# Performance work log

Measured on AMD Instinct MI355X. Metric: run time of the kernel, lower is better.

The kernel has to match this reference:

```python
import jax, jax.numpy as jnp
import numpy as np

# Dimensions pinned by the module: RelPosEmb1DAISummer(tokens=50, dim_head=124)
H = 8          # num_heads
D = 31         # channels // num_heads
T = 4          # time axis of the (p, t) spatial grid; D*T == 124 == dim_head
P = 50         # tokens
C = H * D      # 248 channels
SCALE = D ** -0.5  # note: module scales by d**-0.5 (=31), not (d*t)**-0.5 -- faithful


def rel_to_abs(x):
    """AI-Summer 1D relative->absolute reindexing. x: [b, h, l, 2l-1] -> [b, h, l, l]."""
    b, h, l, _ = x.shape
    x = jnp.pad(x, ((0, 0), (0, 0), (0, 0), (0, 1)))          # [b,h,l,2l]
    x = x.reshape(b, h, l * 2 * l)
    x = jnp.pad(x, ((0, 0), (0, 0), (0, l - 1)))
    x = x.reshape(b, h, l + 1, 2 * l - 1)
    return x[:, :, :l, l - 1:]


def setup_inputs() -> dict:
    key = jax.random.key(0)
    k1, k2, k3, k4 = jax.random.split(key, 4)
    B = 512
    x = jax.random.normal(k1, (B, C, P, T), jnp.float32)
    # 1x1 conv == per-position linear over channels: weight [3C, C], bias [3C]
    w_qkv = jax.random.normal(k2, (3 * C, C), jnp.float32) * (C ** -0.5)
    b_qkv = jax.random.normal(k3, (3 * C,), jnp.float32) * 0.01
    # shared-heads relative position embedding: [2*tokens-1, dim_head]
    rel_emb = jax.random.normal(k4, (2 * P - 1, D * T), jnp.float32) * ((D * T) ** -0.5)
    return {"x": x, "w_qkv": w_qkv, "b_qkv": b_qkv, "rel_emb": rel_emb}


def reference(x, w_qkv, b_qkv, rel_emb):
    B = x.shape[0]
    # 1x1 Conv2d: [B, C, P, T] -> [B, 3C, P, T]
    qkv = jnp.einsum('bcpt,oc->bopt', x, w_qkv) + b_qkv[None, :, None, None]
    # 'b (qkv h d) p t -> qkv b h d p t'
    qkv = qkv.reshape(B, 3, H, D, P, T)
    q, k, v = qkv[:, 0], qkv[:, 1], qkv[:, 2]                 # each [B,H,D,P,T]
    q = q.transpose(0, 1, 3, 2, 4).reshape(B, H, P, D * T)    # 'b h d p t -> b h p (d t)'
    k = k.transpose(0, 1, 2, 4, 3).reshape(B, H, D * T, P)    # 'b h d p t -> b h (d t) p'
    v = v.transpose(0, 1, 3, 2, 4).reshape(B, H, P, D * T)
    dots = jnp.einsum('bhpi,bhiq->bhpq', q, k)                # [B,H,P,P]
    bias = rel_to_abs(jnp.einsum('bhpd,rd->bhpr', q, rel_emb))
    attn = jax.nn.softmax((dots + bias) * SCALE, axis=-1)     # dropout = identity (eval)
    out = jnp.einsum('bhpq,bhqi->bhpi', attn, v)              # [B,H,P,D*T]
    # 'b h p (d t) -> b (h d) p t'
    out = out.reshape(B, H, P, D, T).transpose(0, 1, 3, 2, 4).reshape(B, H * D, P, T)
    return out
```

## Files before the change

kernel.cpp:

```cpp
#include <hip/hip_runtime.h>
#include <hip/hip_bf16.h>
#include <stdint.h>

typedef __bf16 bf16_t;
typedef bf16_t bf16x8 __attribute__((ext_vector_type(8)));
typedef bf16_t bf16x4 __attribute__((ext_vector_type(4)));
typedef float f32x4 __attribute__((ext_vector_type(4)));

constexpr float SCALE = 0.17960530202677491f;

__device__ __forceinline__ f32x4 mfma16(bf16x8 a, bf16x8 b, f32x4 c) {
    return __builtin_amdgcn_mfma_f32_16x16x32_bf16(a, b, c, 0, 0, 0);
}
__device__ __forceinline__ void fence() {
    asm volatile("s_waitcnt lgkmcnt(0)" ::: "memory");
}
__device__ __forceinline__ void gload_lds16(const void* g, void* l) {
    __builtin_amdgcn_global_load_lds((const __attribute__((address_space(1))) void*)g,
                                     (__attribute__((address_space(3))) void*)l, 16, 0, 0);
}

__global__ void prep_kernel(const float* __restrict__ w, const float* __restrict__ rel,
                            bf16_t* __restrict__ WT, bf16_t* __restrict__ relf)
{
    int i = blockIdx.x * 256 + threadIdx.x;
    if (i < 196608) {
        int o = i >> 8, c = i & 255;
        WT[i] = (o < 744 && c < 248) ? (bf16_t)w[(long)o * 248 + c] : (bf16_t)0.f;
        return;
    }
    i -= 196608;
    if (i < 14336) {
        int e = i & 7, lane = (i >> 3) & 63;
        int f = i >> 9;
        int ks = f & 3, rt = f >> 2;
        int r = rt * 16 + (lane & 15);
        int dt = ks * 32 + (lane >> 4) * 8 + e;
        float v = 0.f;
        if (r < 99 && dt < 124) v = rel[r * 124 + dt];
        relf[i] = (bf16_t)v;
    }
}

__global__ void __launch_bounds__(512)
xb_kernel(const float* __restrict__ x, bf16_t* __restrict__ XT)
{
    __shared__ __align__(16) char XS[31744];
    const int tid = threadIdx.x;
    const int blk = blockIdx.x;
    const int cl = tid & 63;
    const int cg = tid >> 6;
    {
        int f = blk * 64 + cl;
        int b = f / 200;
        int nn = f - b * 200;
        const float* xp = x + (long)b * 49600 + nn;
#pragma unroll
        for (int ii = 0; ii < 4; ++ii) {
            int cb = cg + 8 * ii;
            if (cb < 31) {
                bf16x8 pk;
#pragma unroll
                for (int e = 0; e < 8; ++e)
                    pk[e] = (bf16_t)xp[(long)(cb * 8 + e) * 200];
                *(bf16x8*)(XS + cl * 496 + cb * 16) = pk;
            }
        }
    }
    __syncthreads();
    if (tid < 496) {
        char* dst = (char*)XT + (long)blk * 31744 + tid * 64;
#pragma unroll
        for (int j = 0; j < 4; ++j)
            *(f32x4*)(dst + j * 16) = *(const f32x4*)(XS + tid * 64 + j * 16);
    }
}

__global__ void __launch_bounds__(256)
qkv_kernel(const bf16_t* __restrict__ XT, const bf16_t* __restrict__ WT,
           const float* __restrict__ bqkv, bf16_t* __restrict__ qk,
           bf16_t* __restrict__ vbuf)
{
    __shared__ __align__(16) char SM[16384];
    const int raw = blockIdx.x;
    const int swz = (raw & 7) * 600 + (raw >> 3);
    const int mt = swz % 6, nt = swz / 6;
    const int n0 = nt * 128, o0 = mt * 128;
    const int tid  = threadIdx.x;
    const int lane = tid & 63;
    const int wv   = tid >> 6;
    const int r15  = lane & 15, g4 = lane >> 4;
    const int kc   = lane & 3, rsub = lane >> 2;
    const int wr = wv >> 1, wc = wv & 1;

    f32x4 acc[4][4];
#pragma unroll
    for (int a = 0; a < 4; ++a)
#pragma unroll
        for (int b = 0; b < 4; ++b) acc[a][b] = f32x4{0.f, 0.f, 0.f, 0.f};

    const char* XTb = (const char*)XT;
    const char* WTb = (const char*)WT;

#define STAGE(BUF, KS)                                                          \
    {                                                                           \
        _Pragma("unroll")                                                       \
        for (int i_ = 0; i_ < 2; ++i_) {                                        \
            int r0 = (wv * 2 + i_) * 16;                                        \
            int row = r0 + rsub;                                                \
            gload_lds16(XTb + (long)(n0 + row) * 496 + ((KS) * 4 + kc) * 16,    \
                        SM + (BUF) * 8192 + r0 * 64);                           \
        }                                                                       \
    }

    STAGE(0, 0);
    __syncthreads();

    int buf = 0;
    for (int ks = 0; ks < 8; ++ks) {
        if (ks < 7) STAGE(buf ^ 1, ks + 1);
        bf16x8 Af[4], Bf[4];
#pragma unroll
        for (int fo = 0; fo < 4; ++fo) {
            int row = wc * 64 + fo * 16 + r15;
            Bf[fo] = *(const bf16x8*)(WTb + (long)(o0 + row) * 512 + (ks * 4 + g4) * 16);
        }
#pragma unroll
        for (int fn = 0; fn < 4; ++fn) {
            int row = wr * 64 + fn * 16 + r15;
            Af[fn] = *(const bf16x8*)(SM + buf * 8192 + row * 64 + g4 * 16);
        }
#pragma unroll
        for (int fn = 0; fn < 4; ++fn)
#pragma unroll
            for (int fo = 0; fo < 4; ++fo)
                acc[fn][fo] = mfma16(Af[fn], Bf[fo], acc[fn][fo]);
        __syncthreads();
        buf ^= 1;
    }
#undef STAGE

#pragma unroll
    for (int fo = 0; fo < 4; ++fo) {
        int o = o0 + wc * 64 + fo * 16 + r15;
        bool vo = (o < 744);
        int s = (o >= 496) ? 2 : ((o >= 248) ? 1 : 0);
        int rem = o - s * 248;
        int h = rem / 31;
        int d = rem - h * 31;
        float bias = vo ? bqkv[o] : 0.f;
        float sc = (s == 0) ? SCALE : 1.f;
#pragma unroll
        for (int fn = 0; fn < 4; ++fn) {
            int n = n0 + wr * 64 + fn * 16 + g4 * 4;
            int b = n / 200;
            int p = (n - b * 200) >> 2;
            long bh = (long)(b * 8 + h);
            if (vo) {
                f32x4 a = acc[fn][fo];
                bf16x4 pk = {(bf16_t)((a[0] + bias) * sc), (bf16_t)((a[1] + bias) * sc),
                             (bf16_t)((a[2] + bias) * sc), (bf16_t)((a[3] + bias) * sc)};
                if (s < 2)
                    *(bf16x4*)(qk + (long)s * 26214400 + (bh * 50 + p) * 128 + d * 4) = pk;
                else
                    *(bf16x4*)(vbuf + bh * 8192 + p * 128 + d * 4) = pk;
            }
        }
    }
}

__global__ void __launch_bounds__(256)
attn_kernel(const bf16_t* __restrict__ qk, const bf16_t* __restrict__ vbuf,
            const bf16_t* __restrict__ relf, float* __restrict__ out)
{
    __shared__ float LS[50][52];
    __shared__ __align__(16) char AS[8192];
    __shared__ __align__(16) char VT[16384];
    __shared__ float RS[64];
    const int bid = blockIdx.x;
    const int bb = bid >> 3, hh = bid & 7;
    const int tid  = threadIdx.x;
    const int lane = tid & 63;
    const int w    = tid >> 6;
    const int r15  = lane & 15, g4 = lane >> 4;

    const bf16_t* qB = qk + (long)bid * 6400;
    const bf16_t* kB = qk + 26214400L + (long)bid * 6400;
    const bf16_t* vB = vbuf + (long)bid * 8192;

    {
        int p_ = tid >> 2, cc = tid & 3;
#pragma unroll
        for (int u = 0; u < 4; ++u) {
            int c = cc + u * 4;
            bf16x8 vv = *(const bf16x8*)(vB + p_ * 128 + c * 8);
#pragma unroll
            for (int e = 0; e < 8; ++e) {
                int i = c * 8 + e;
                *(bf16_t*)(VT + i * 128 + (((p_ >> 3) ^ (i & 7)) << 4) + (p_ & 7) * 2) = vv[e];
            }
        }
    }

    bf16x8 Afr[4];
#pragma unroll
    for (int ks = 0; ks < 4; ++ks)
        Afr[ks] = *(const bf16x8*)(qB + (w * 16 + r15) * 128 + ks * 32 + g4 * 8);

#pragma unroll
    for (int ct = 0; ct < 4; ++ct) {
        int c = ct * 16 + r15;
        f32x4 sA = f32x4{0.f, 0.f, 0.f, 0.f};
#pragma unroll
        for (int ks = 0; ks < 4; ++ks) {
            bf16x8 Bf = *(const bf16x8*)(kB + c * 128 + ks * 32 + g4 * 8);
            sA = mfma16(Afr[ks], Bf, sA);
        }
        if (c < 50) {
#pragma unroll
            for (int j = 0; j < 4; ++j) {
                int qrow = w * 16 + g4 * 4 + j;
                if (qrow < 50) LS[qrow][c] = sA[j];
            }
        }
    }
    fence();

    {
        const int rt0 = (w < 2) ? (2 - w) : 0;
        const int rt1 = 6 - w;
        const bf16_t* rf = relf + lane * 8;
        for (int rt = rt0; rt <= rt1; ++rt) {
            bf16x8 R[4];
#pragma unroll
            for (int ks = 0; ks < 4; ++ks)
                R[ks] = *(const bf16x8*)(rf + ((rt * 4 + ks) << 9));
            f32x4 sA = f32x4{0.f, 0.f, 0.f, 0.f};
#pragma unroll
            for (int ks = 0; ks < 4; ++ks) sA = mfma16(Afr[ks], R[ks], sA);
            int r = rt * 16 + r15;
#pragma unroll
            for (int j = 0; j < 4; ++j) {
                int qrow = w * 16 + g4 * 4 + j;
                int jj = r + qrow - 49;
                if (qrow < 50 && jj >= 0 && jj < 50) LS[qrow][jj] += sA[j];
            }
        }
    }
    fence();

    {
        int row = w * 16 + (lane >> 2);
        int quad = lane & 3;
        int hrow = row & 7;
        if (row < 50) {
            float mx = -1e30f;
            for (int jj = quad; jj < 50; jj += 4) mx = fmaxf(mx, LS[row][jj]);
            mx = fmaxf(mx, __shfl_xor(mx, 1));
            mx = fmaxf(mx, __shfl_xor(mx, 2));
            float sum = 0.f;
            for (int jj = quad; jj < 50; jj += 4) {
                float e = __expf(LS[row][jj] - mx);
                sum += e;
                *(bf16_t*)(AS + row * 128 + (((jj >> 3) ^ hrow) << 4) + (jj & 7) * 2) = (bf16_t)e;
            }
            for (int jj = 50 + quad; jj < 64; jj += 4)
                *(bf16_t*)(AS + row * 128 + (((jj >> 3) ^ hrow) << 4) + (jj & 7) * 2) = (bf16_t)0.f;
            sum += __shfl_xor(sum, 1);
            sum += __shfl_xor(sum, 2);
            if (quad == 0) RS[row] = 1.f / sum;
        } else {
            for (int jj = quad; jj < 64; jj += 4)
                *(bf16_t*)(AS + row * 128 + (((jj >> 3) ^ hrow) << 4) + (jj & 7) * 2) = (bf16_t)0.f;
        }
    }
    __syncthreads();

#pragma unroll
    for (int ii = 0; ii < 2; ++ii) {
        int itile = w * 2 + ii;
        int irow = itile * 16 + r15;
        bf16x8 Av[2];
#pragma unroll
        for (int ks = 0; ks < 2; ++ks)
            Av[ks] = *(const bf16x8*)(VT + irow * 128 + ((((ks << 2) | g4) ^ (irow & 7)) << 4));
        int dd = itile * 4 + g4;
#pragma unroll
        for (int pt = 0; pt < 4; ++pt) {
            int prow = pt * 16 + r15;
            int hp2 = prow & 7;
            f32x4 po = f32x4{0.f, 0.f, 0.f, 0.f};
#pragma unroll
            for (int ks = 0; ks < 2; ++ks) {
                bf16x8 Bs = *(const bf16x8*)(AS + prow * 128 + ((((ks << 2) | g4) ^ hp2) << 4));
                po = mfma16(Av[ks], Bs, po);
            }
            if (dd < 31 && prow < 50) {
                float rsv = RS[prow];
                po[0] *= rsv; po[1] *= rsv; po[2] *= rsv; po[3] *= rsv;
                *(f32x4*)(out + ((long)bb * 248 + hh * 31 + dd) * 200 + prow * 4) = po;
            }
        }
    }
}

extern "C" void kernel_launch(void* const* d_in, const int* in_sizes, int n_in,
                              void* d_out, int out_size, void* d_ws, size_t ws_size,
                              hipStream_t stream)
{
    const float* x   = (const float*)d_in[0];
    const float* wq  = (const float*)d_in[1];
    const float* bq  = (const float*)d_in[2];
    const float* rel = (const float*)d_in[3];
    float* out = (float*)d_out;

    char* ws = (char*)d_ws;
    bf16_t* WT   = (bf16_t*)ws;
    bf16_t* relf = (bf16_t*)(ws + 393216);
    bf16_t* qk   = (bf16_t*)(ws + 421888);
    bf16_t* vbuf = qk + 52428800L;

    bf16_t* XT = (bf16_t*)d_out;

    const int B = in_sizes[0] / 49600;

    prep_kernel<<<dim3(824), dim3(256), 0, stream>>>(wq, rel, WT, relf);
    xb_kernel<<<dim3(B * 200 / 64), dim3(512), 0, stream>>>(x, XT);
    qkv_kernel<<<dim3(4800), dim3(256), 0, stream>>>(XT, WT, bq, qk, vbuf);
    attn_kernel<<<dim3(B * 8), dim3(256), 0, stream>>>(qk, vbuf, relf, out);
}
```

Before: 232.4 us.

## Retile QKV GEMM to load full-K X tile once with swizzled LDS

The QKV projection GEMM now uses 64x256 tiles instead of 128x128. Each block loads its full-K X strip (64 rows x 512 bytes) into LDS once, with an XOR swizzle to avoid bank conflicts. This removes the per-k-step double buffering and barriers. Weight fragments are register-prefetched one k-step ahead from global, and each wave covers 64 output channels across all 64 rows. The change trades larger LDS use (32KB) and possibly lower occupancy for fewer syncs and less reloading of X.

```diff
diff --git a/kernel.cpp b/kernel.cpp
--- a/kernel.cpp
+++ b/kernel.cpp
@@ -81,68 +81,66 @@
            const float* __restrict__ bqkv, bf16_t* __restrict__ qk,
            bf16_t* __restrict__ vbuf)
 {
-    __shared__ __align__(16) char SM[16384];
-    const int raw = blockIdx.x;
-    const int swz = (raw & 7) * 600 + (raw >> 3);
-    const int mt = swz % 6, nt = swz / 6;
-    const int n0 = nt * 128, o0 = mt * 128;
+    __shared__ __align__(16) char SM[32768];
+    const int blk = blockIdx.x;
+    const int ntile = blk / 3, ot = blk - ntile * 3;
+    const int n0 = ntile * 64, o0 = ot * 256;
     const int tid  = threadIdx.x;
     const int lane = tid & 63;
     const int wv   = tid >> 6;
     const int r15  = lane & 15, g4 = lane >> 4;
-    const int kc   = lane & 3, rsub = lane >> 2;
-    const int wr = wv >> 1, wc = wv & 1;
-
-    f32x4 acc[4][4];
-#pragma unroll
-    for (int a = 0; a < 4; ++a)
-#pragma unroll
-        for (int b = 0; b < 4; ++b) acc[a][b] = f32x4{0.f, 0.f, 0.f, 0.f};
 
     const char* XTb = (const char*)XT;
     const char* WTb = (const char*)WT;
 
-#define STAGE(BUF, KS)                                                          \
-    {                                                                           \
-        _Pragma("unroll")                                                       \
-        for (int i_ = 0; i_ < 2; ++i_) {                                        \
-            int r0 = (wv * 2 + i_) * 16;                                        \
-            int row = r0 + rsub;                                                \
-            gload_lds16(XTb + (long)(n0 + row) * 496 + ((KS) * 4 + kc) * 16,    \
-                        SM + (BUF) * 8192 + r0 * 64);                           \
-        }                                                                       \
-    }
-
-    STAGE(0, 0);
+#pragma unroll
+    for (int s = 0; s < 8; ++s) {
+        int idx = s * 256 + tid;
+        int row = idx >> 5;
+        int cL  = idx & 31;
+        int cS  = cL ^ (row & 31);
+        gload_lds16(XTb + (long)(n0 + row) * 496 + cS * 16,
+                    SM + ((s * 256 + (tid & ~63)) << 4));
+    }
     __syncthreads();
 
-    int buf = 0;
+    f32x4 acc[4][4];
+#pragma unroll
+    for (int a = 0; a < 4; ++a)
+#pragma unroll
+        for (int b = 0; b < 4; ++b) acc[a][b] = f32x4{0.f, 0.f, 0.f, 0.f};
+
+    const char* wB = WTb + (long)(o0 + wv * 64 + r15) * 512;
+    bf16x8 Bc[4], Bn[4];
+#pragma unroll
+    for (int fo = 0; fo < 4; ++fo)
+        Bc[fo] = *(const bf16x8*)(wB + fo * 16 * 512 + g4 * 16);
+
     for (int ks = 0; ks < 8; ++ks) {
-        if (ks < 7) STAGE(buf ^ 1, ks + 1);
-        bf16x8 Af[4], Bf[4];
-#pragma unroll
-        for (int fo = 0; fo < 4; ++fo) {
-            int row = wc * 64 + fo * 16 + r15;
-            Bf[fo] = *(const bf16x8*)(WTb + (long)(o0 + row) * 512 + (ks * 4 + g4) * 16);
-        }
+        if (ks < 7) {
+#pragma unroll
+            for (int fo = 0; fo < 4; ++fo)
+                Bn[fo] = *(const bf16x8*)(wB + fo * 16 * 512 + ((ks + 1) * 4 + g4) * 16);
+        }
+        bf16x8 Af[4];
 #pragma unroll
         for (int fn = 0; fn < 4; ++fn) {
-            int row = wr * 64 + fn * 16 + r15;
-            Af[fn] = *(const bf16x8*)(SM + buf * 8192 + row * 64 + g4 * 16);
+            int row = fn * 16 + r15;
+            int cL = (ks * 4 + g4) ^ (row & 31);
+            Af[fn] = *(const bf16x8*)(SM + row * 512 + cL * 16);
         }
 #pragma unroll
         for (int fn = 0; fn < 4; ++fn)
 #pragma unroll
             for (int fo = 0; fo < 4; ++fo)
-                acc[fn][fo] = mfma16(Af[fn], Bf[fo], acc[fn][fo]);
-        __syncthreads();
-        buf ^= 1;
-    }
-#undef STAGE
+                acc[fn][fo] = mfma16(Af[fn], Bc[fo], acc[fn][fo]);
+#pragma unroll
+        for (int fo = 0; fo < 4; ++fo) Bc[fo] = Bn[fo];
+    }
 
 #pragma unroll
     for (int fo = 0; fo < 4; ++fo) {
-        int o = o0 + wc * 64 + fo * 16 + r15;
+        int o = o0 + wv * 64 + fo * 16 + r15;
         bool vo = (o < 744);
         int s = (o >= 496) ? 2 : ((o >= 248) ? 1 : 0);
         int rem = o - s * 248;
@@ -152,7 +150,7 @@
         float sc = (s == 0) ? SCALE : 1.f;
 #pragma unroll
         for (int fn = 0; fn < 4; ++fn) {
-            int n = n0 + wr * 64 + fn * 16 + g4 * 4;
+            int n = n0 + fn * 16 + g4 * 4;
             int b = n / 200;
             int p = (n - b * 200) >> 2;
             long bh = (long)(b * 8 + h);
```

After: 233.5 us. About the same (+0.5%).
